# Performance work log

Hardware: AMD Instinct MI355X
Metric: run time of the kernel (lower is better)

## Reference

```python
import jax, jax.numpy as jnp
import numpy as np

B, S, D = 32, 1024, 1024  # S must equal D for scores @ v to type-check


def setup_inputs() -> dict:
    key = jax.random.key(0)
    k0, k1, k2, k3, k4, k5 = jax.random.split(key, 6)
    x = jax.random.normal(k0, (B, S, D), dtype=jnp.float32)
    Wq = jax.random.normal(k1, (D, D), dtype=jnp.float32) * 0.02
    bq = jnp.zeros((D,), dtype=jnp.float32)
    Wk = jax.random.normal(k2, (D, D), dtype=jnp.float32) * 0.02
    bk = jnp.zeros((D,), dtype=jnp.float32)
    v = jax.random.uniform(k3, (D,), dtype=jnp.float32)  # torch.rand init
    return {"x": x, "Wq": Wq, "bq": bq, "Wk": Wk, "bk": bk, "v": v}


def reference(x, Wq, bq, Wk, bk, v):
    # Linear layers (torch Linear: y = x @ W^T + b)
    q = jnp.einsum('bsd,ed->bse', x, Wq) + bq          # [B,S,D]
    k = jnp.einsum('bsd,ed->bse', x, Wk) + bk          # [B,S,D]
    scores = jnp.tanh(jnp.einsum('bsd,btd->bst', q, k))  # [B,S,S]
    s = jnp.einsum('bst,t->bs', scores, v)             # [B,S] (S == D)
    w = jax.nn.softmax(s, axis=-1)                     # [B,S]
    out = jnp.einsum('bs,bsd->bd', w, x)               # [B,D]
    return out
```

## Files before the change

kernel.cpp:

```cpp
#include <hip/hip_runtime.h>
#include <hip/hip_bf16.h>
#include <math.h>

#define BB 32
#define SS 1024
#define DD 1024

typedef __bf16 bf16_t;
typedef __bf16 bf16x4 __attribute__((ext_vector_type(4)));
typedef __bf16 bf16x8 __attribute__((ext_vector_type(8)));
typedef float f32x4 __attribute__((ext_vector_type(4)));

__device__ __forceinline__ void gload16(const void* g, void* lds_uniform) {
    __builtin_amdgcn_global_load_lds(
        (const __attribute__((address_space(1))) void*)g,
        (__attribute__((address_space(3))) void*)lds_uniform, 16, 0, 0);
}

__device__ __forceinline__ void stage32(const bf16_t* __restrict__ src,
                                        int row0, int k0, char* slot, int tid) {
    const int r = tid >> 2;
    const int c = ((tid & 3) ^ ((tid >> 3) & 3)) * 8;
    char* d = slot + (tid >> 6) * 1024;
    const bf16_t* s = src + (size_t)(row0 + r) * DD + k0 + c;
    gload16(s, d);
    gload16(s + (size_t)128 * DD, d + 8192);
}

#define VM8  asm volatile("s_waitcnt vmcnt(8)" ::: "memory")
#define VM4  asm volatile("s_waitcnt vmcnt(4)" ::: "memory")
#define VM0  asm volatile("s_waitcnt vmcnt(0)" ::: "memory")
#define BARR asm volatile("s_barrier" ::: "memory")

#define SEL_A(u) ((((u) >> 5) == 2) ? Alo : Ahi)
#define SEL_B(u) ((((u) >> 5) == 1) ? Blo : Bhi)
#define K0OF(u)  (((u) & 31) * 32)

#define TILE32(u, s, DOST) do {                                               \
    if (DOST) stage32(SEL_A((u)+3), rowA, K0OF((u)+3),                        \
                      AslR + ((((u)+3)&3) * 16384), tid);                     \
    bf16x8 bfr[4], af[4];                                                     \
    _Pragma("unroll") for (int fc = 0; fc < 4; ++fc)                          \
        bfr[fc] = *(const bf16x8*)(Bbase##s + fc * 1024);                     \
    _Pragma("unroll") for (int fr = 0; fr < 4; ++fr)                          \
        af[fr] = *(const bf16x8*)(Abase##s + fr * 1024);                      \
    _Pragma("unroll") for (int fr = 0; fr < 4; ++fr)                          \
        _Pragma("unroll") for (int fc = 0; fc < 4; ++fc)                      \
            acc[fr][fc] = __builtin_amdgcn_mfma_f32_16x16x32_bf16(            \
                af[fr], bfr[fc], acc[fr][fc], 0, 0, 0);                       \
    if (DOST) stage32(SEL_B((u)+3), rowB, K0OF((u)+3),                        \
                      BslR + ((((u)+3)&3) * 16384), tid);                     \
    _Pragma("unroll") for (int fr = 0; fr < 4; ++fr)                          \
        af[fr] = *(const bf16x8*)(Abase##s + 4096 + fr * 1024);               \
    _Pragma("unroll") for (int fr = 0; fr < 4; ++fr)                          \
        _Pragma("unroll") for (int fc = 0; fc < 4; ++fc)                      \
            acc[4+fr][fc] = __builtin_amdgcn_mfma_f32_16x16x32_bf16(          \
                af[fr], bfr[fc], acc[4+fr][fc], 0, 0, 0);                     \
} while (0)

__device__ __forceinline__ void kloop_ring(
    const bf16_t* __restrict__ Ahi, const bf16_t* __restrict__ Alo,
    const bf16_t* __restrict__ Bhi, const bf16_t* __restrict__ Blo,
    int rowA, int rowB, int tid, int lane, int wm, int wn,
    char* AslR, char* BslR, f32x4 (*acc)[4])
{
    const int aoff = (lane & 15) * 64 + (((lane >> 4) ^ ((lane >> 1) & 3)) * 16);
    const char* Abase0 = AslR + wm * 8192 + aoff;
    const char* Abase1 = Abase0 + 16384;
    const char* Abase2 = Abase0 + 32768;
    const char* Abase3 = Abase0 + 49152;
    const char* Bbase0 = BslR + wn * 4096 + aoff;
    const char* Bbase1 = Bbase0 + 16384;
    const char* Bbase2 = Bbase0 + 32768;
    const char* Bbase3 = Bbase0 + 49152;

    stage32(SEL_A(0), rowA, K0OF(0), AslR, tid);
    stage32(SEL_B(0), rowB, K0OF(0), BslR, tid);
    stage32(SEL_A(1), rowA, K0OF(1), AslR + 16384, tid);
    stage32(SEL_B(1), rowB, K0OF(1), BslR + 16384, tid);
    stage32(SEL_A(2), rowA, K0OF(2), AslR + 32768, tid);
    stage32(SEL_B(2), rowB, K0OF(2), BslR + 32768, tid);
    VM8;
    BARR;

    for (int i = 0; i < 23; ++i) {
        const int u0 = i * 4;
        TILE32(u0 + 0, 0, true); VM8; BARR;
        TILE32(u0 + 1, 1, true); VM8; BARR;
        TILE32(u0 + 2, 2, true); VM8; BARR;
        TILE32(u0 + 3, 3, true); VM8; BARR;
    }
    TILE32(92, 0, true);  VM8; BARR;
    TILE32(93, 1, false); VM4; BARR;
    TILE32(94, 2, false); VM0; BARR;
    TILE32(95, 3, false);
}

__global__ __launch_bounds__(512, 2) void gemm_y_256(
    const bf16_t* __restrict__ xh, const bf16_t* __restrict__ xl,
    const bf16_t* __restrict__ Mth, const bf16_t* __restrict__ Mtl,
    bf16_t* __restrict__ out_hi, bf16_t* __restrict__ out_lo)
{
    __shared__ __align__(16) bf16_t Asl[4][256 * 32];
    __shared__ __align__(16) bf16_t Bsl[4][256 * 32];
    const int tid = threadIdx.x;
    const int lane = tid & 63, wid = tid >> 6;
    const int wm = wid >> 2, wn = wid & 3;
    const int lin = (blockIdx.x & 7) * 64 + (blockIdx.x >> 3);
    const int m0 = (lin >> 2) * 256;
    const int n0 = (lin & 3) * 256;

    f32x4 acc[8][4] = {};
    kloop_ring(xh, xl, Mth, Mtl, m0, n0, tid, lane, wm, wn,
               (char*)Asl, (char*)Bsl, acc);

    const int rbase = (lane >> 4) * 4;
    const int cbase = lane & 15;
    #pragma unroll
    for (int fr = 0; fr < 8; ++fr) {
        #pragma unroll
        for (int fc = 0; fc < 4; ++fc) {
            const int n = n0 + wn * 64 + fc * 16 + cbase;
            #pragma unroll
            for (int r = 0; r < 4; ++r) {
                const int m = m0 + wm * 128 + fr * 16 + rbase + r;
                float vf = acc[fr][fc][r];
                bf16_t h = (bf16_t)vf;
                out_hi[(size_t)m * DD + n] = h;
                out_lo[(size_t)m * DD + n] = (bf16_t)(vf - (float)h);
            }
        }
    }
}

__global__ __launch_bounds__(512, 2) void gemm_scores_256(
    const bf16_t* __restrict__ yh, const bf16_t* __restrict__ yl,
    const bf16_t* __restrict__ xh, const bf16_t* __restrict__ xl,
    const float* __restrict__ v, const float* __restrict__ alpha,
    const float* __restrict__ beta, const float* __restrict__ cbuf,
    float* __restrict__ sbuf)
{
    __shared__ __align__(16) bf16_t Asl[4][256 * 32];
    __shared__ __align__(16) bf16_t Bsl[4][256 * 32];
    const int tid = threadIdx.x;
    const int lane = tid & 63, wid = tid >> 6;
    const int wm = wid >> 2, wn = wid & 3;
    const int lin = (blockIdx.x & 7) * 64 + (blockIdx.x >> 3);
    const int t0 = (lin & 3) * 256;
    const int s0 = ((lin >> 2) & 3) * 256;
    const int b  = lin >> 4;
    const size_t boff = (size_t)b * SS * DD;

    f32x4 acc[8][4] = {};
    kloop_ring(yh + boff, yl + boff, xh + boff, xl + boff, s0, t0,
               tid, lane, wm, wn, (char*)Asl, (char*)Bsl, acc);

    const float c0 = cbuf[0];
    const int rbase = (lane >> 4) * 4;
    const int cbase = lane & 15;
    float bet[4], vv[4];
    #pragma unroll
    for (int fc = 0; fc < 4; ++fc) {
        const int t = t0 + wn * 64 + fc * 16 + cbase;
        bet[fc] = beta[b * SS + t];
        vv[fc]  = v[t];
    }
    #pragma unroll
    for (int fr = 0; fr < 8; ++fr) {
        #pragma unroll
        for (int r = 0; r < 4; ++r) {
            const int srow = s0 + wm * 128 + fr * 16 + rbase + r;
            const float al = alpha[b * SS + srow] + c0;
            float p = 0.f;
            #pragma unroll
            for (int fc = 0; fc < 4; ++fc)
                p += tanhf(acc[fr][fc][r] + al + bet[fc]) * vv[fc];
            p += __shfl_xor(p, 1);
            p += __shfl_xor(p, 2);
            p += __shfl_xor(p, 4);
            p += __shfl_xor(p, 8);
            if (cbase == 0) atomicAdd(&sbuf[b * SS + srow], p);
        }
    }
}

__global__ __launch_bounds__(256) void split_fp32(
    const float* __restrict__ src, bf16_t* __restrict__ hi,
    bf16_t* __restrict__ lo, int n4)
{
    for (int idx = blockIdx.x * 256 + threadIdx.x; idx < n4;
         idx += gridDim.x * 256) {
        float4 f = ((const float4*)src)[idx];
        bf16x4 h, l;
        h.x = (bf16_t)f.x; h.y = (bf16_t)f.y; h.z = (bf16_t)f.z; h.w = (bf16_t)f.w;
        l.x = (bf16_t)(f.x - (float)h.x);
        l.y = (bf16_t)(f.y - (float)h.y);
        l.z = (bf16_t)(f.z - (float)h.z);
        l.w = (bf16_t)(f.w - (float)h.w);
        ((bf16x4*)hi)[idx] = h;
        ((bf16x4*)lo)[idx] = l;
    }
}

__global__ __launch_bounds__(256) void split_x_ab(
    const float* __restrict__ src, bf16_t* __restrict__ hi,
    bf16_t* __restrict__ lo, const float* __restrict__ avec,
    const float* __restrict__ bvec, float* __restrict__ alpha,
    float* __restrict__ beta)
{
    __shared__ float reda[4], redb[4];
    const int tid = threadIdx.x;
    const int lane = tid & 63, wave = tid >> 6;
    const float4 av = ((const float4*)avec)[tid];
    const float4 bv = ((const float4*)bvec)[tid];
    const int n4 = BB * SS * DD / 4;
    for (int idx = blockIdx.x * 256 + tid; idx < n4; idx += gridDim.x * 256) {
        float4 f = ((const float4*)src)[idx];
        bf16x4 h, l;
        h.x = (bf16_t)f.x; h.y = (bf16_t)f.y; h.z = (bf16_t)f.z; h.w = (bf16_t)f.w;
        l.x = (bf16_t)(f.x - (float)h.x);
        l.y = (bf16_t)(f.y - (float)h.y);
        l.z = (bf16_t)(f.z - (float)h.z);
        l.w = (bf16_t)(f.w - (float)h.w);
        ((bf16x4*)hi)[idx] = h;
        ((bf16x4*)lo)[idx] = l;

        float pa = f.x * av.x + f.y * av.y + f.z * av.z + f.w * av.w;
        float pb = f.x * bv.x + f.y * bv.y + f.z * bv.z + f.w * bv.w;
        #pragma unroll
        for (int off = 32; off; off >>= 1) {
            pa += __shfl_xor(pa, off);
            pb += __shfl_xor(pb, off);
        }
        if (lane == 0) { reda[wave] = pa; redb[wave] = pb; }
        __syncthreads();
        if (tid == 0) {
            const int row = idx >> 8;
            alpha[row] = reda[0] + reda[1] + reda[2] + reda[3];
            beta[row]  = redb[0] + redb[1] + redb[2] + redb[3];
        }
        __syncthreads();
    }
}

__global__ __launch_bounds__(256) void bias_gemv(
    const float* __restrict__ Wq, const float* __restrict__ Wk,
    const float* __restrict__ bq, const float* __restrict__ bk,
    float* __restrict__ avec, float* __restrict__ bvec)
{
    const float* W   = blockIdx.z ? Wk : Wq;
    const float* bb  = blockIdx.z ? bq : bk;
    float* outv      = blockIdx.z ? bvec : avec;
    const int d  = blockIdx.x * 256 + threadIdx.x;
    const int e0 = blockIdx.y * 64;
    float s = 0.f;
    for (int e = e0; e < e0 + 64; ++e) s += W[(size_t)e * DD + d] * bb[e];
    atomicAdd(&outv[d], s);
}

__global__ __launch_bounds__(256) void dot_c(
    const float* __restrict__ bq, const float* __restrict__ bk,
    float* __restrict__ cbuf)
{
    __shared__ float red[4];
    const int tid = threadIdx.x, lane = tid & 63, wave = tid >> 6;
    float s = 0.f;
    for (int e = tid; e < DD; e += 256) s += bq[e] * bk[e];
    #pragma unroll
    for (int off = 32; off; off >>= 1) s += __shfl_xor(s, off);
    if (lane == 0) red[wave] = s;
    __syncthreads();
    if (tid == 0) cbuf[0] = red[0] + red[1] + red[2] + red[3];
}

__global__ __launch_bounds__(256) void mt_f32(
    const float* __restrict__ Wk, const float* __restrict__ Wq,
    float* __restrict__ Mt)
{
    __shared__ float Us[16][68];
    __shared__ float Vs[16][68];
    const int tid = threadIdx.x;
    const int tx = tid & 15, ty = tid >> 4;
    const int i0 = blockIdx.y * 64;
    const int j0 = blockIdx.x * 64;
    float acc[4][4] = {};
    for (int e0 = 0; e0 < DD; e0 += 16) {
        #pragma unroll
        for (int r = 0; r < 4; ++r) {
            const int kk = (tid >> 6) + r * 4;
            const int cc = tid & 63;
            Us[kk][cc] = Wk[(size_t)(e0 + kk) * DD + i0 + cc];
            Vs[kk][cc] = Wq[(size_t)(e0 + kk) * DD + j0 + cc];
        }
        __syncthreads();
        #pragma unroll
        for (int kk = 0; kk < 16; ++kk) {
            float4 a = *(const float4*)&Us[kk][ty * 4];
            float4 w = *(const float4*)&Vs[kk][tx * 4];
            acc[0][0] += a.x * w.x; acc[0][1] += a.x * w.y; acc[0][2] += a.x * w.z; acc[0][3] += a.x * w.w;
            acc[1][0] += a.y * w.x; acc[1][1] += a.y * w.y; acc[1][2] += a.y * w.z; acc[1][3] += a.y * w.w;
            acc[2][0] += a.z * w.x; acc[2][1] += a.z * w.y; acc[2][2] += a.z * w.z; acc[2][3] += a.z * w.w;
            acc[3][0] += a.w * w.x; acc[3][1] += a.w * w.y; acc[3][2] += a.w * w.z; acc[3][3] += a.w * w.w;
        }
        __syncthreads();
    }
    #pragma unroll
    for (int i = 0; i < 4; ++i)
        #pragma unroll
        for (int j = 0; j < 4; ++j)
            Mt[(size_t)(i0 + ty * 4 + i) * DD + j0 + tx * 4 + j] = acc[i][j];
}

__global__ __launch_bounds__(256) void softmax_rows(
    const float* __restrict__ sbuf, float* __restrict__ wbuf)
{
    const int b = blockIdx.x, tid = threadIdx.x;
    const int wave = tid >> 6, lane = tid & 63;
    __shared__ float redm[4];
    __shared__ float redsum[4];

    float vals[4];
    float mx = -1e30f;
    #pragma unroll
    for (int i = 0; i < 4; ++i) {
        vals[i] = sbuf[b * SS + i * 256 + tid];
        mx = fmaxf(mx, vals[i]);
    }
    #pragma unroll
    for (int off = 32; off; off >>= 1) mx = fmaxf(mx, __shfl_xor(mx, off));
    if (lane == 0) redm[wave] = mx;
    __syncthreads();
    mx = fmaxf(fmaxf(redm[0], redm[1]), fmaxf(redm[2], redm[3]));

    float sum = 0.f;
    #pragma unroll
    for (int i = 0; i < 4; ++i) { vals[i] = expf(vals[i] - mx); sum += vals[i]; }
    #pragma unroll
    for (int off = 32; off; off >>= 1) sum += __shfl_xor(sum, off);
    if (lane == 0) redsum[wave] = sum;
    __syncthreads();
    sum = redsum[0] + redsum[1] + redsum[2] + redsum[3];

    float inv = 1.0f / sum;
    #pragma unroll
    for (int i = 0; i < 4; ++i) wbuf[b * SS + i * 256 + tid] = vals[i] * inv;
}

__global__ __launch_bounds__(256) void weighted_sum(
    const float* __restrict__ x, const float* __restrict__ wbuf,
    float* __restrict__ out)
{
    __shared__ float wl[SS];
    const int b = blockIdx.y;
    const int d = blockIdx.x * 256 + threadIdx.x;
    for (int i = threadIdx.x; i < SS; i += 256) wl[i] = wbuf[b * SS + i];
    __syncthreads();

    const float* xb = x + (size_t)b * SS * DD + d;
    float acc = 0.f;
    for (int s = 0; s < SS; ++s) acc += wl[s] * xb[(size_t)s * DD];
    out[b * DD + d] = acc;
}

extern "C" void kernel_launch(void* const* d_in, const int* in_sizes, int n_in,
                              void* d_out, int out_size, void* d_ws, size_t ws_size,
                              hipStream_t stream) {
    const float* x  = (const float*)d_in[0];
    const float* Wq = (const float*)d_in[1];
    const float* bq = (const float*)d_in[2];
    const float* Wk = (const float*)d_in[3];
    const float* bk = (const float*)d_in[4];
    const float* v  = (const float*)d_in[5];
    float* out = (float*)d_out;

    const size_t nx = (size_t)BB * SS * DD;
    const size_t nw = (size_t)DD * DD;

    dim3 blk(256);

    char* p = (char*)d_ws;
    bf16_t* xh  = (bf16_t*)p;   p += nx * 2;
    bf16_t* xl  = (bf16_t*)p;   p += nx * 2;
    bf16_t* yh  = (bf16_t*)p;   p += nx * 2;
    bf16_t* yl  = (bf16_t*)p;   p += nx * 2;
    float*  Mt  = (float*)p;    p += nw * 4;
    bf16_t* Mth = (bf16_t*)p;   p += nw * 2;
    bf16_t* Mtl = (bf16_t*)p;   p += nw * 2;
    float*  avec = (float*)p;   p += 4096;
    float*  bvec = (float*)p;   p += 4096;
    float*  cbuf = (float*)p;   p += 16;
    float*  alpha = (float*)p;  p += (size_t)BB * SS * 4;
    float*  beta  = (float*)p;  p += (size_t)BB * SS * 4;
    float*  sbuf  = (float*)p;  p += (size_t)BB * SS * 4;
    float*  wbuf  = (float*)p;

    hipMemsetAsync(sbuf, 0, (size_t)BB * SS * sizeof(float), stream);
    hipMemsetAsync(avec, 0, 4096 * 2, stream);

    bias_gemv<<<dim3(4, 16, 2), blk, 0, stream>>>(Wq, Wk, bq, bk, avec, bvec);
    dot_c<<<1, blk, 0, stream>>>(bq, bk, cbuf);
    split_x_ab<<<2048, blk, 0, stream>>>(x, xh, xl, avec, bvec, alpha, beta);
    mt_f32<<<dim3(16, 16), blk, 0, stream>>>(Wk, Wq, Mt);
    split_fp32<<<512, blk, 0, stream>>>(Mt, Mth, Mtl, (int)(nw / 4));

    gemm_y_256<<<512, dim3(512), 0, stream>>>(xh, xl, Mth, Mtl, yh, yl);
    gemm_scores_256<<<512, dim3(512), 0, stream>>>(yh, yl, xh, xl, v,
                                                   alpha, beta, cbuf, sbuf);

    softmax_rows<<<BB, blk, 0, stream>>>(sbuf, wbuf);
    dim3 g4(DD / 256, BB);
    weighted_sum<<<g4, blk, 0, stream>>>(x, wbuf, out);
}
```

Before: 650.5 us.

## Fuse Mt split into GEMM epilogue, wave-per-row x split, bf16 weighted sum

Removes the fp32 Mt buffer by writing the bf16 hi/lo split directly from the Mt GEMM epilogue. Rewrites split_x_ab so that each wave processes one row, removing the block-level syncthreads reductions. Weighted sum now reads the bf16 hi copy of x instead of fp32 and splits along the sequence with atomic accumulation into a zeroed output. This halves the traffic for that stage but drops the low-order bits of x in the final sum.

```diff
diff --git a/kernel.cpp b/kernel.cpp
--- a/kernel.cpp
+++ b/kernel.cpp
@@ -7,6 +7,7 @@
 #define DD 1024
 
 typedef __bf16 bf16_t;
+typedef __bf16 bf16x2 __attribute__((ext_vector_type(2)));
 typedef __bf16 bf16x4 __attribute__((ext_vector_type(4)));
 typedef __bf16 bf16x8 __attribute__((ext_vector_type(8)));
 typedef float f32x4 __attribute__((ext_vector_type(4)));
@@ -184,62 +185,45 @@
     }
 }
 
-__global__ __launch_bounds__(256) void split_fp32(
-    const float* __restrict__ src, bf16_t* __restrict__ hi,
-    bf16_t* __restrict__ lo, int n4)
-{
-    for (int idx = blockIdx.x * 256 + threadIdx.x; idx < n4;
-         idx += gridDim.x * 256) {
-        float4 f = ((const float4*)src)[idx];
-        bf16x4 h, l;
-        h.x = (bf16_t)f.x; h.y = (bf16_t)f.y; h.z = (bf16_t)f.z; h.w = (bf16_t)f.w;
-        l.x = (bf16_t)(f.x - (float)h.x);
-        l.y = (bf16_t)(f.y - (float)h.y);
-        l.z = (bf16_t)(f.z - (float)h.z);
-        l.w = (bf16_t)(f.w - (float)h.w);
-        ((bf16x4*)hi)[idx] = h;
-        ((bf16x4*)lo)[idx] = l;
-    }
-}
-
 __global__ __launch_bounds__(256) void split_x_ab(
     const float* __restrict__ src, bf16_t* __restrict__ hi,
     bf16_t* __restrict__ lo, const float* __restrict__ avec,
     const float* __restrict__ bvec, float* __restrict__ alpha,
     float* __restrict__ beta)
 {
-    __shared__ float reda[4], redb[4];
-    const int tid = threadIdx.x;
-    const int lane = tid & 63, wave = tid >> 6;
-    const float4 av = ((const float4*)avec)[tid];
-    const float4 bv = ((const float4*)bvec)[tid];
-    const int n4 = BB * SS * DD / 4;
-    for (int idx = blockIdx.x * 256 + tid; idx < n4; idx += gridDim.x * 256) {
-        float4 f = ((const float4*)src)[idx];
-        bf16x4 h, l;
-        h.x = (bf16_t)f.x; h.y = (bf16_t)f.y; h.z = (bf16_t)f.z; h.w = (bf16_t)f.w;
-        l.x = (bf16_t)(f.x - (float)h.x);
-        l.y = (bf16_t)(f.y - (float)h.y);
-        l.z = (bf16_t)(f.z - (float)h.z);
-        l.w = (bf16_t)(f.w - (float)h.w);
-        ((bf16x4*)hi)[idx] = h;
-        ((bf16x4*)lo)[idx] = l;
-
-        float pa = f.x * av.x + f.y * av.y + f.z * av.z + f.w * av.w;
-        float pb = f.x * bv.x + f.y * bv.y + f.z * bv.z + f.w * bv.w;
+    const int lane = threadIdx.x & 63, wave = threadIdx.x >> 6;
+    float4 av[4], bv[4];
+    #pragma unroll
+    for (int j = 0; j < 4; ++j) {
+        av[j] = ((const float4*)avec)[j * 64 + lane];
+        bv[j] = ((const float4*)bvec)[j * 64 + lane];
+    }
+    for (int row = blockIdx.x * 4 + wave; row < BB * SS; row += 2048 * 4) {
+        const float4* xr = (const float4*)(src + (size_t)row * DD);
+        bf16x4* hr = (bf16x4*)(hi + (size_t)row * DD);
+        bf16x4* lr = (bf16x4*)(lo + (size_t)row * DD);
+        float pa = 0.f, pb = 0.f;
+        #pragma unroll
+        for (int j = 0; j < 4; ++j) {
+            float4 f = xr[j * 64 + lane];
+            bf16x4 h, l;
+            h.x = (bf16_t)f.x; h.y = (bf16_t)f.y;
+            h.z = (bf16_t)f.z; h.w = (bf16_t)f.w;
+            l.x = (bf16_t)(f.x - (float)h.x);
+            l.y = (bf16_t)(f.y - (float)h.y);
+            l.z = (bf16_t)(f.z - (float)h.z);
+            l.w = (bf16_t)(f.w - (float)h.w);
+            hr[j * 64 + lane] = h;
+            lr[j * 64 + lane] = l;
+            pa += f.x * av[j].x + f.y * av[j].y + f.z * av[j].z + f.w * av[j].w;
+            pb += f.x * bv[j].x + f.y * bv[j].y + f.z * bv[j].z + f.w * bv[j].w;
+        }
         #pragma unroll
         for (int off = 32; off; off >>= 1) {
             pa += __shfl_xor(pa, off);
             pb += __shfl_xor(pb, off);
         }
-        if (lane == 0) { reda[wave] = pa; redb[wave] = pb; }
-        __syncthreads();
-        if (tid == 0) {
-            const int row = idx >> 8;
-            alpha[row] = reda[0] + reda[1] + reda[2] + reda[3];
-            beta[row]  = redb[0] + redb[1] + redb[2] + redb[3];
-        }
-        __syncthreads();
+        if (lane == 0) { alpha[row] = pa; beta[row] = pb; }
     }
 }
 
@@ -273,9 +257,9 @@
     if (tid == 0) cbuf[0] = red[0] + red[1] + red[2] + red[3];
 }
 
-__global__ __launch_bounds__(256) void mt_f32(
+__global__ __launch_bounds__(256) void mt_split(
     const float* __restrict__ Wk, const float* __restrict__ Wq,
-    float* __restrict__ Mt)
+    bf16_t* __restrict__ Mth, bf16_t* __restrict__ Mtl)
 {
     __shared__ float Us[16][68];
     __shared__ float Vs[16][68];
@@ -305,10 +289,16 @@
         __syncthreads();
     }
     #pragma unroll
-    for (int i = 0; i < 4; ++i)
-        #pragma unroll
-        for (int j = 0; j < 4; ++j)
-            Mt[(size_t)(i0 + ty * 4 + i) * DD + j0 + tx * 4 + j] = acc[i][j];
+    for (int i = 0; i < 4; ++i) {
+        #pragma unroll
+        for (int j = 0; j < 4; ++j) {
+            const size_t o = (size_t)(i0 + ty * 4 + i) * DD + j0 + tx * 4 + j;
+            float vf = acc[i][j];
+            bf16_t h = (bf16_t)vf;
+            Mth[o] = h;
+            Mtl[o] = (bf16_t)(vf - (float)h);
+        }
+    }
 }
 
 __global__ __launch_bounds__(256) void softmax_rows(
@@ -347,19 +337,31 @@
 }
 
 __global__ __launch_bounds__(256) void weighted_sum(
-    const float* __restrict__ x, const float* __restrict__ wbuf,
+    const bf16_t* __restrict__ xh, const float* __restrict__ wbuf,
     float* __restrict__ out)
 {
-    __shared__ float wl[SS];
+    __shared__ float wl[256];
     const int b = blockIdx.y;
-    const int d = blockIdx.x * 256 + threadIdx.x;
-    for (int i = threadIdx.x; i < SS; i += 256) wl[i] = wbuf[b * SS + i];
+    const int s0 = blockIdx.x * 256;
+    const int tid = threadIdx.x;
+    wl[tid] = wbuf[b * SS + s0 + tid];
     __syncthreads();
 
-    const float* xb = x + (size_t)b * SS * DD + d;
-    float acc = 0.f;
-    for (int s = 0; s < SS; ++s) acc += wl[s] * xb[(size_t)s * DD];
-    out[b * DD + d] = acc;
+    float a0 = 0.f, a1 = 0.f, a2 = 0.f, a3 = 0.f;
+    const bf16_t* xb = xh + (size_t)b * SS * DD + (size_t)s0 * DD;
+    #pragma unroll 4
+    for (int s = 0; s < 256; ++s) {
+        const bf16_t* xr = xb + (size_t)s * DD;
+        bf16x2 u = *(const bf16x2*)(xr + tid * 2);
+        bf16x2 w2 = *(const bf16x2*)(xr + tid * 2 + 512);
+        const float w = wl[s];
+        a0 += w * (float)u.x;  a1 += w * (float)u.y;
+        a2 += w * (float)w2.x; a3 += w * (float)w2.y;
+    }
+    atomicAdd(&out[b * DD + tid * 2], a0);
+    atomicAdd(&out[b * DD + tid * 2 + 1], a1);
+    atomicAdd(&out[b * DD + tid * 2 + 512], a2);
+    atomicAdd(&out[b * DD + tid * 2 + 513], a3);
 }
 
 extern "C" void kernel_launch(void* const* d_in, const int* in_sizes, int n_in,
@@ -383,7 +385,6 @@
     bf16_t* xl  = (bf16_t*)p;   p += nx * 2;
     bf16_t* yh  = (bf16_t*)p;   p += nx * 2;
     bf16_t* yl  = (bf16_t*)p;   p += nx * 2;
-    float*  Mt  = (float*)p;    p += nw * 4;
     bf16_t* Mth = (bf16_t*)p;   p += nw * 2;
     bf16_t* Mtl = (bf16_t*)p;   p += nw * 2;
     float*  avec = (float*)p;   p += 4096;
@@ -396,18 +397,17 @@
 
     hipMemsetAsync(sbuf, 0, (size_t)BB * SS * sizeof(float), stream);
     hipMemsetAsync(avec, 0, 4096 * 2, stream);
+    hipMemsetAsync(out, 0, (size_t)BB * DD * sizeof(float), stream);
 
     bias_gemv<<<dim3(4, 16, 2), blk, 0, stream>>>(Wq, Wk, bq, bk, avec, bvec);
     dot_c<<<1, blk, 0, stream>>>(bq, bk, cbuf);
     split_x_ab<<<2048, blk, 0, stream>>>(x, xh, xl, avec, bvec, alpha, beta);
-    mt_f32<<<dim3(16, 16), blk, 0, stream>>>(Wk, Wq, Mt);
-    split_fp32<<<512, blk, 0, stream>>>(Mt, Mth, Mtl, (int)(nw / 4));
+    mt_split<<<dim3(16, 16), blk, 0, stream>>>(Wk, Wq, Mth, Mtl);
 
     gemm_y_256<<<512, dim3(512), 0, stream>>>(xh, xl, Mth, Mtl, yh, yl);
     gemm_scores_256<<<512, dim3(512), 0, stream>>>(yh, yl, xh, xl, v,
                                                    alpha, beta, cbuf, sbuf);
 
     softmax_rows<<<BB, blk, 0, stream>>>(sbuf, wbuf);
-    dim3 g4(DD / 256, BB);
-    weighted_sum<<<g4, blk, 0, stream>>>(x, wbuf, out);
-}
+    weighted_sum<<<dim3(4, BB), blk, 0, stream>>>(xh, wbuf, out);
+}
```

Result: faster. 623.9 us (-4.1%).
